# Kernel optimization log

Hardware: AMD Instinct MI355X
Metric: run time of the kernel (lower is better)

Reference implementation:

```python
import jax, jax.numpy as jnp
import numpy as np

B, N, M, D, NH, HD = 2, 1024, 1024, 1536, 16, 96
RD = HD // 3  # per-axis rotary dim = 32
EPS = 1e-6
SCALE = HD ** -0.5


def _rmsnorm(y, w):
    return y * jax.lax.rsqrt(jnp.mean(y * y, axis=-1, keepdims=True) + EPS) * w


def _rope_tables(T, H, W):
    # inv_freqs identical for t/h/w since all three dims are RD
    inv_f = 1.0 / (10000.0 ** (jnp.arange(0, RD, 2, dtype=jnp.float32)[: RD // 2] / RD))
    gt, gh, gw = jnp.meshgrid(
        jnp.arange(T, dtype=jnp.float32),
        jnp.arange(H, dtype=jnp.float32),
        jnp.arange(W, dtype=jnp.float32),
        indexing='ij')
    ft = gt.reshape(-1, 1) * inv_f[None, :]  # [L, RD//2]
    fh = gh.reshape(-1, 1) * inv_f[None, :]
    fw = gw.reshape(-1, 1) * inv_f[None, :]
    return (jnp.cos(ft), jnp.sin(ft), jnp.cos(fh), jnp.sin(fh), jnp.cos(fw), jnp.sin(fw))


def _apply_rope(xq, cos, sin):
    # xq: [B, L, NH, RD]; cos/sin: [L, RD//2]
    c = jnp.concatenate([cos, cos], axis=-1)[None, :, None, :]
    s = jnp.concatenate([sin, sin], axis=-1)[None, :, None, :]
    x1, x2 = jnp.split(xq, 2, axis=-1)
    rot = jnp.concatenate([-x2, x1], axis=-1)
    return xq * c + rot * s


def setup_inputs() -> dict:
    key = jax.random.key(0)
    ks = jax.random.split(key, 10)
    w = lambda k: jax.random.normal(k, (D, D), dtype=jnp.float32) * 0.02
    return {
        'cond': jax.random.normal(ks[0], (B, N, D), dtype=jnp.float32),
        'x': jax.random.normal(ks[1], (B, M, D), dtype=jnp.float32),
        'cond_q_w': w(ks[2]), 'cond_k_w': w(ks[3]), 'cond_v_w': w(ks[4]),
        'cond_qnorm_w': jnp.ones((D,), jnp.float32),
        'cond_knorm_w': jnp.ones((D,), jnp.float32),
        'cond_proj_w': w(ks[5]),
        'x_q_w': w(ks[6]), 'x_k_w': w(ks[7]), 'x_v_w': w(ks[8]),
        'x_qnorm_w': jnp.ones((D,), jnp.float32),
        'x_knorm_w': jnp.ones((D,), jnp.float32),
        'x_proj_w': w(ks[9]),
        'T': 2, 'H': 32, 'W': 32,
    }


def reference(cond, x, cond_q_w, cond_k_w, cond_v_w, cond_qnorm_w, cond_knorm_w,
              cond_proj_w, x_q_w, x_k_w, x_v_w, x_qnorm_w, x_knorm_w, x_proj_w,
              T, H, W):
    # dual-stream QKV + RMSNorm (qkv_bias=False, eval -> no dropout)
    cq = _rmsnorm(cond @ cond_q_w, cond_qnorm_w).reshape(B, N, NH, HD)
    ck = _rmsnorm(cond @ cond_k_w, cond_knorm_w).reshape(B, N, NH, HD)
    cv = (cond @ cond_v_w).reshape(B, N, NH, HD)
    xq = _rmsnorm(x @ x_q_w, x_qnorm_w).reshape(B, M, NH, HD)
    xk = _rmsnorm(x @ x_k_w, x_knorm_w).reshape(B, M, NH, HD)
    xv = (x @ x_v_w).reshape(B, M, NH, HD)

    q = jnp.concatenate([cq, xq], axis=1)  # [B, N+M, NH, HD]
    k = jnp.concatenate([ck, xk], axis=1)
    v = jnp.concatenate([cv, xv], axis=1)

    # 3D RoPE: split head_dim into t/h/w thirds and rotate each with its own freqs
    cos_t, sin_t, cos_h, sin_h, cos_w, sin_w = _rope_tables(T, H, W)
    qt, qh, qw = jnp.split(q, 3, axis=-1)
    kt, kh, kw = jnp.split(k, 3, axis=-1)
    q = jnp.concatenate([_apply_rope(qt, cos_t, sin_t),
                         _apply_rope(qh, cos_h, sin_h),
                         _apply_rope(qw, cos_w, sin_w)], axis=-1)
    k = jnp.concatenate([_apply_rope(kt, cos_t, sin_t),
                         _apply_rope(kh, cos_h, sin_h),
                         _apply_rope(kw, cos_w, sin_w)], axis=-1)

    # joint non-causal SDPA
    scores = jnp.einsum('blhd,bmhd->bhlm', q, k) * SCALE
    attn = jax.nn.softmax(scores, axis=-1)
    out = jnp.einsum('bhlm,bmhd->blhd', attn, v).reshape(B, N + M, D)

    cond_out = out[:, :N] @ cond_proj_w
    x_out = out[:, N:] @ x_proj_w
    return cond_out, x_out
```

## Files before the change

### kernel.cpp

```cpp
#include <hip/hip_runtime.h>
#include <stdint.h>

#define DEV __device__ __forceinline__

using f32x4  = __attribute__((ext_vector_type(4))) float;
using f32x16 = __attribute__((ext_vector_type(16))) float;
using bf16x8 = __attribute__((ext_vector_type(8))) short;

DEV ushort f2bf(float f){
  uint32_t u = __float_as_uint(f);
  u += 0x7FFFu + ((u >> 16) & 1u);
  return (ushort)(u >> 16);
}
DEV float bf2f(ushort h){ return __uint_as_float(((uint32_t)h) << 16); }

DEV void async16(const void* g, void* l){
  __builtin_amdgcn_global_load_lds(
      (const __attribute__((address_space(1))) void*)g,
      (__attribute__((address_space(3))) void*)l, 16, 0, 0);
}

union FU { uint4 u; bf16x8 v; };
DEV bf16x8 as_bf16x8(uint a, uint b, uint c, uint d){ FU f; f.u = make_uint4(a,b,c,d); return f.v; }

__global__ __launch_bounds__(256) void k_conv_in(const float* __restrict__ src, ushort* __restrict__ dst){
  int i = (blockIdx.x * 256 + threadIdx.x) * 8;
  float4 a = *(const float4*)(src + i);
  float4 b = *(const float4*)(src + i + 4);
  union { ushort s[8]; uint4 q; } o;
  o.s[0]=f2bf(a.x); o.s[1]=f2bf(a.y); o.s[2]=f2bf(a.z); o.s[3]=f2bf(a.w);
  o.s[4]=f2bf(b.x); o.s[5]=f2bf(b.y); o.s[6]=f2bf(b.z); o.s[7]=f2bf(b.w);
  *(uint4*)(dst + i) = o.q;
}

__global__ __launch_bounds__(256) void k_transpose_w(
    const float* w0, const float* w1, const float* w2, const float* w3,
    const float* w4, const float* w5, const float* w6, const float* w7,
    ushort* __restrict__ dst){
  __shared__ float tile[32][33];
  int z = blockIdx.z;
  const float* src = (z==0)?w0:(z==1)?w1:(z==2)?w2:(z==3)?w3:(z==4)?w4:(z==5)?w5:(z==6)?w6:w7;
  int n0 = blockIdx.x * 32;
  int k0 = blockIdx.y * 32;
  int tx = threadIdx.x;
  int ty = threadIdx.y;
  for (int j = 0; j < 4; ++j)
    tile[ty + j*8][tx] = src[(size_t)(k0 + ty + j*8) * 1536 + n0 + tx];
  __syncthreads();
  ushort* d = dst + (size_t)z * 1536 * 1536;
  for (int j = 0; j < 4; ++j){
    int n = n0 + ty + j*8;
    int k = k0 + tx;
    d[(size_t)n * 1536 + k] = f2bf(tile[tx][ty + j*8]);
  }
}

template<bool OUT_BF16>
DEV void gemm_tile(const ushort* __restrict__ A, const ushort* __restrict__ Bt, void* __restrict__ Cp,
                   int K, int lda, int ldb, int ldc, int m0, int n0){
  __shared__ ushort As[8192];
  __shared__ ushort Bs[8192];
  int tid = threadIdx.x;
  int w = tid >> 6, lane = tid & 63;
  int g = lane >> 4, fr = lane & 15;
  int wm = (w >> 1) * 64, wn = (w & 1) * 64;
  f32x4 acc[4][4] = {};
  for (int kt = 0; kt < K; kt += 64){
    __syncthreads();
#pragma unroll
    for (int i = 0; i < 4; ++i){
      int ci = i * 256 + tid;
      int row = ci >> 3, ch = ci & 7;
      int src8 = (ch ^ (row & 7)) * 8;
      async16(A  + (size_t)(m0 + row) * lda + kt + src8, As + (i*256 + w*64) * 8);
      async16(Bt + (size_t)(n0 + row) * ldb + kt + src8, Bs + (i*256 + w*64) * 8);
    }
    __syncthreads();
#pragma unroll
    for (int ks = 0; ks < 2; ++ks){
      bf16x8 af[4], bf[4];
      int cidx = ((ks*4 + g) ^ (fr & 7)) * 8;
#pragma unroll
      for (int mi = 0; mi < 4; ++mi) af[mi] = *(const bf16x8*)(As + (wm + mi*16 + fr) * 64 + cidx);
#pragma unroll
      for (int ni = 0; ni < 4; ++ni) bf[ni] = *(const bf16x8*)(Bs + (wn + ni*16 + fr) * 64 + cidx);
#pragma unroll
      for (int mi = 0; mi < 4; ++mi)
#pragma unroll
        for (int ni = 0; ni < 4; ++ni)
          acc[mi][ni] = __builtin_amdgcn_mfma_f32_16x16x32_bf16(af[mi], bf[ni], acc[mi][ni], 0, 0, 0);
    }
  }
  int cr = (lane >> 4) * 4, cc2 = lane & 15;
#pragma unroll
  for (int mi = 0; mi < 4; ++mi)
#pragma unroll
    for (int ni = 0; ni < 4; ++ni)
#pragma unroll
      for (int r = 0; r < 4; ++r){
        size_t idx = (size_t)(m0 + wm + mi*16 + cr + r) * ldc + (n0 + wn + ni*16 + cc2);
        if (OUT_BF16) ((ushort*)Cp)[idx] = f2bf(acc[mi][ni][r]);
        else          ((float*)Cp)[idx]  = acc[mi][ni][r];
      }
}

__global__ __launch_bounds__(256) void k_gemm_qkv(const ushort* __restrict__ inb, const ushort* __restrict__ Wt,
                                                  ushort* __restrict__ Y){
  int f = blockIdx.x;
  int nid = (f & 7) * 144 + (f >> 3);
  int z = nid / 576; int rr = nid - z * 576;
  int by = rr / 36;  int bx = rr - by * 36;
  gemm_tile<true>(inb + (size_t)z * 2048 * 1536, Wt + (size_t)z * 4608 * 1536,
                  Y + (size_t)z * 2048 * 4608, 1536, 1536, 1536, 4608,
                  by * 128, bx * 128);
}

__global__ __launch_bounds__(256) void k_gemm_proj(const ushort* __restrict__ AO, const ushort* __restrict__ Wtp,
                                                   float* __restrict__ out){
  int f = blockIdx.x;
  int nid = (f & 7) * 48 + (f >> 3);
  int z = nid / 96; int rr = nid - z * 96;
  int by = rr / 12; int bx = rr - by * 12;
  int s = z >> 1, bb = z & 1;
  gemm_tile<false>(AO + (size_t)(bb*2048 + s*1024) * 1536, Wtp + (size_t)s * 1536 * 1536,
                   (void*)(out + (size_t)(s*2048 + bb*1024) * 1536), 1536, 1536, 1536, 1536,
                   by * 128, bx * 128);
}

__global__ __launch_bounds__(256) void k_norm_rope(
    const ushort* __restrict__ Y,
    const float* __restrict__ qn_c, const float* __restrict__ kn_c,
    const float* __restrict__ qn_x, const float* __restrict__ kn_x,
    ushort* __restrict__ Qb, ushort* __restrict__ Kb, ushort* __restrict__ Vb){
  int r = blockIdx.x;
  int z = blockIdx.y;
  const ushort* y = Y + ((size_t)z * 2048 + r) * 4608;
  const float* qw = z ? qn_x : qn_c;
  const float* kw = z ? kn_x : kn_c;
  int b = r >> 10;
  int l = (z << 10) + (r & 1023);
  int tid = threadIdx.x;
  __shared__ float cs[48], sn[48];
  if (tid < 48){
    int axis = tid >> 4, fj = tid & 15;
    int pos = (axis == 0) ? (l >> 10) : ((axis == 1) ? ((l >> 5) & 31) : (l & 31));
    float inv = __expf(-(float)fj * 0.5756462732485114f);
    float a = (float)pos * inv;
    sn[tid] = sinf(a); cs[tid] = cosf(a);
  }
  float yq1[3], yq2[3], yk1[3], yk2[3];
  float ssq = 0.f, ssk = 0.f;
#pragma unroll
  for (int i = 0; i < 3; ++i){
    int p = tid + i*256;
    int head = p / 48, rem = p % 48;
    int c1 = head*96 + (rem >> 4)*32 + (rem & 15);
    float a1 = bf2f(y[c1]),        a2 = bf2f(y[c1 + 16]);
    float b1 = bf2f(y[1536 + c1]), b2 = bf2f(y[1536 + c1 + 16]);
    yq1[i]=a1; yq2[i]=a2; yk1[i]=b1; yk2[i]=b2;
    ssq += a1*a1 + a2*a2;
    ssk += b1*b1 + b2*b2;
  }
#pragma unroll
  for (int mm = 1; mm < 64; mm <<= 1){
    ssq += __shfl_xor(ssq, mm);
    ssk += __shfl_xor(ssk, mm);
  }
  __shared__ float red[8];
  int w = tid >> 6;
  if ((tid & 63) == 0){ red[w] = ssq; red[4 + w] = ssk; }
  __syncthreads();
  float scq = rsqrtf((red[0]+red[1]+red[2]+red[3]) * (1.f/1536.f) + 1e-6f);
  float sck = rsqrtf((red[4]+red[5]+red[6]+red[7]) * (1.f/1536.f) + 1e-6f);
  float scqS = scq * 0.1020620726159658f;
#pragma unroll
  for (int i = 0; i < 3; ++i){
    int p = tid + i*256;
    int head = p / 48, rem = p % 48;
    int axis = rem >> 4, fj = rem & 15;
    int c1 = head*96 + axis*32 + fj;
    float c = cs[rem], s = sn[rem];
    size_t rowb = ((size_t)(b*16 + head) * 2048 + l) * 96;
    float a1 = yq1[i] * scqS * qw[c1], a2 = yq2[i] * scqS * qw[c1 + 16];
    Qb[rowb + axis*32 + fj]      = f2bf(a1*c - a2*s);
    Qb[rowb + axis*32 + fj + 16] = f2bf(a2*c + a1*s);
    float b1 = yk1[i] * sck * kw[c1], b2 = yk2[i] * sck * kw[c1 + 16];
    int d1 = axis*32 + fj;
    Kb[rowb + d1]      = f2bf(b1*c - b2*s);
    Kb[rowb + d1 + 16] = f2bf(b2*c + b1*s);
  }
#pragma unroll
  for (int i = 0; i < 6; ++i){
    int cidx = tid + i*256;
    int head = cidx / 96, hd = cidx - head*96;
    Vb[((size_t)(b*16 + head) * 2048 + l) * 96 + hd] = y[3072 + cidx];
  }
}

__global__ __launch_bounds__(256) void k_transpose_v(const ushort* __restrict__ V, ushort* __restrict__ Vt){
  __shared__ ushort t[32][33];
  int bh = blockIdx.z;
  const ushort* src = V + (size_t)bh * 2048 * 96;
  ushort* dst = Vt + (size_t)bh * 96 * 2048;
  int c0 = blockIdx.x * 32;
  int r0 = blockIdx.y * 32;
  int tx = threadIdx.x, ty = threadIdx.y;
  for (int j = 0; j < 4; ++j)
    t[ty + j*8][tx] = src[(size_t)(r0 + ty + j*8) * 96 + c0 + tx];
  __syncthreads();
  for (int j = 0; j < 4; ++j){
    int d = c0 + ty + j*8;
    int l = r0 + tx;
    dst[(size_t)d * 2048 + l] = t[tx][ty + j*8];
  }
}

__global__ __launch_bounds__(256, 2) void k_attn(const ushort* __restrict__ Qb, const ushort* __restrict__ Kb,
                                                 const ushort* __restrict__ Vt, ushort* __restrict__ AO){
  __shared__ ushort Ks[64*100];
  __shared__ ushort Vs[96*68];
  int id = blockIdx.x;
  int nid = (id & 7) * 64 + (id >> 3);
  int qt = nid & 15, bh = nid >> 4;
  int b = bh >> 4, head = bh & 15;
  const ushort* Qh = Qb + (size_t)bh * 2048 * 96;
  const ushort* Kh = Kb + (size_t)bh * 2048 * 96;
  const ushort* Vh = Vt + (size_t)bh * 96 * 2048;
  int tid = threadIdx.x;
  int w = tid >> 6, lane = tid & 63;
  int h = lane >> 5, c = lane & 31;
  int q0 = qt * 128 + w * 32;

  bf16x8 qf[6];
#pragma unroll
  for (int kb = 0; kb < 6; ++kb)
    qf[kb] = *(const bf16x8*)(Qh + (size_t)(q0 + c) * 96 + kb*16 + h*8);

  int gko[3], lko[3], gvo[3], lvo[3];
#pragma unroll
  for (int i = 0; i < 3; ++i){
    int fc = i*256 + tid;
    int krow = (fc * 683) >> 13;
    int kc8  = (fc - krow*12) * 8;
    gko[i] = krow*96 + kc8;
    lko[i] = krow*100 + kc8;
    int vrow = fc >> 3;
    int vc8  = (fc & 7) * 8;
    gvo[i] = vrow*2048 + vc8;
    lvo[i] = vrow*68 + (vc8 ^ ((vrow & 7) << 3));
  }
  uint4 kst[3], vst[3];
#pragma unroll
  for (int i = 0; i < 3; ++i){
    kst[i] = *(const uint4*)(Kh + gko[i]);
    vst[i] = *(const uint4*)(Vh + (size_t)gvo[i]);
  }

  f32x16 o[3] = {};
  float dpart = 0.f;

  for (int kt = 0; kt < 32; ++kt){
#pragma unroll
    for (int i = 0; i < 3; ++i){
      *(uint2*)(Ks + lko[i])     = make_uint2(kst[i].x, kst[i].y);
      *(uint2*)(Ks + lko[i] + 4) = make_uint2(kst[i].z, kst[i].w);
      *(uint2*)(Vs + lvo[i])     = make_uint2(vst[i].x, vst[i].y);
      *(uint2*)(Vs + lvo[i] + 4) = make_uint2(vst[i].z, vst[i].w);
    }
    if (kt + 1 < 32){
#pragma unroll
      for (int i = 0; i < 3; ++i){
        kst[i] = *(const uint4*)(Kh + (kt+1)*6144 + gko[i]);
        vst[i] = *(const uint4*)(Vh + (kt+1)*64 + (size_t)gvo[i]);
      }
    }
    asm volatile("s_waitcnt lgkmcnt(0)" ::: "memory");
    __builtin_amdgcn_s_barrier();
    asm volatile("" ::: "memory");

#pragma unroll
    for (int ni = 0; ni < 2; ++ni){
      f32x16 sa = {};
#pragma unroll
      for (int kb = 0; kb < 6; ++kb){
        const ushort* kp = Ks + (ni*32 + c)*100 + kb*16 + h*8;
        uint2 lo = *(const uint2*)kp;
        uint2 hi = *(const uint2*)(kp + 4);
        sa = __builtin_amdgcn_mfma_f32_32x32x16_bf16(as_bf16x8(lo.x, lo.y, hi.x, hi.y), qf[kb], sa, 0, 0, 0);
      }
      float p[16];
#pragma unroll
      for (int e = 0; e < 16; ++e){
        float x = fmaf(sa[e], 1.44269504f, -14.4269504f);
        asm("v_exp_f32 %0, %1" : "=v"(p[e]) : "v"(x));
      }
      dpart += (((p[0]+p[1])+(p[2]+p[3])) + ((p[4]+p[5])+(p[6]+p[7])))
             + (((p[8]+p[9])+(p[10]+p[11])) + ((p[12]+p[13])+(p[14]+p[15])));
      uint u[8];
#pragma unroll
      for (int e = 0; e < 8; ++e)
        asm("v_cvt_pk_bf16_f32 %0, %1, %2" : "=v"(u[e]) : "v"(p[2*e]), "v"(p[2*e+1]));
      asm("v_permlane32_swap_b32 %0, %1" : "+v"(u[0]), "+v"(u[2]));
      asm("v_permlane32_swap_b32 %0, %1" : "+v"(u[1]), "+v"(u[3]));
      asm("v_permlane32_swap_b32 %0, %1" : "+v"(u[4]), "+v"(u[6]));
      asm("v_permlane32_swap_b32 %0, %1" : "+v"(u[5]), "+v"(u[7]));
      bf16x8 pf0 = as_bf16x8(u[0], u[1], u[2], u[3]);
      bf16x8 pf1 = as_bf16x8(u[4], u[5], u[6], u[7]);
#pragma unroll
      for (int dt = 0; dt < 3; ++dt){
#pragma unroll
        for (int ks = 0; ks < 2; ++ks){
          int chunk = 4*ni + 2*ks + h;
          const ushort* vp = Vs + (dt*32 + c)*68 + ((chunk ^ (c & 7)) << 3);
          uint2 lo = *(const uint2*)vp;
          uint2 hi = *(const uint2*)(vp + 4);
          o[dt] = __builtin_amdgcn_mfma_f32_32x32x16_bf16(ks ? pf1 : pf0,
                    as_bf16x8(lo.x, lo.y, hi.x, hi.y), o[dt], 0, 0, 0);
        }
      }
    }
    asm volatile("" ::: "memory");
    __builtin_amdgcn_s_barrier();
    asm volatile("" ::: "memory");
  }

  float dtot = dpart + __shfl_xor(dpart, 32);
#pragma unroll
  for (int r = 0; r < 16; ++r){
    int qloc = (r & 3) + 8*(r >> 2) + 4*h;
    float den = __shfl(dtot, qloc);
    float dinv = __builtin_amdgcn_rcpf(den);
    size_t rowoff = ((size_t)b * 2048 + q0 + qloc) * 1536 + head * 96;
#pragma unroll
    for (int dt = 0; dt < 3; ++dt){
      float val = o[dt][r] * dinv;
      uint pk; asm("v_cvt_pk_bf16_f32 %0, %1, %2" : "=v"(pk) : "v"(val), "v"(val));
      AO[rowoff + dt*32 + c] = (ushort)pk;
    }
  }
}

extern "C" void kernel_launch(void* const* d_in, const int* in_sizes, int n_in,
                              void* d_out, int out_size, void* d_ws, size_t ws_size,
                              hipStream_t stream){
  const float* cond = (const float*)d_in[0];
  const float* x    = (const float*)d_in[1];
  const float* wq_c = (const float*)d_in[2];
  const float* wk_c = (const float*)d_in[3];
  const float* wv_c = (const float*)d_in[4];
  const float* qn_c = (const float*)d_in[5];
  const float* kn_c = (const float*)d_in[6];
  const float* wp_c = (const float*)d_in[7];
  const float* wq_x = (const float*)d_in[8];
  const float* wk_x = (const float*)d_in[9];
  const float* wv_x = (const float*)d_in[10];
  const float* qn_x = (const float*)d_in[11];
  const float* kn_x = (const float*)d_in[12];
  const float* wp_x = (const float*)d_in[13];

  char* ws = (char*)d_ws;
  ushort* inb = (ushort*)(ws);
  ushort* Wt  = (ushort*)(ws + 12582912ll);
  ushort* Y   = (ushort*)(ws + 50331648ll);
  ushort* Vt  = (ushort*)(ws + 50331648ll);
  ushort* Qb  = (ushort*)(ws + 88080384ll);
  ushort* Kb  = (ushort*)(ws + 100663296ll);
  ushort* Vb  = (ushort*)(ws + 113246208ll);
  ushort* AO  = inb;

  k_conv_in<<<1536, 256, 0, stream>>>(cond, inb);
  k_conv_in<<<1536, 256, 0, stream>>>(x, inb + 3145728);
  k_transpose_w<<<dim3(48,48,8), dim3(32,8), 0, stream>>>(wq_c, wk_c, wv_c, wq_x, wk_x, wv_x, wp_c, wp_x, Wt);
  k_gemm_qkv<<<1152, 256, 0, stream>>>(inb, Wt, Y);
  k_norm_rope<<<dim3(2048,2), 256, 0, stream>>>(Y, qn_c, kn_c, qn_x, kn_x, Qb, Kb, Vb);
  k_transpose_v<<<dim3(3,64,32), dim3(32,8), 0, stream>>>(Vb, Vt);
  k_attn<<<512, 256, 0, stream>>>(Qb, Kb, Vt, AO);
  k_gemm_proj<<<384, 256, 0, stream>>>(AO, Wt + (size_t)9216*1536, (float*)d_out);
  (void)in_sizes; (void)n_in; (void)out_size; (void)ws_size;
}
```

Baseline: 224.4 us.

## Rewrite QKV GEMM with 256x288 tiles, double-buffered LDS and interleaved prefetch

```diff
diff --git a/kernel.cpp b/kernel.cpp
--- a/kernel.cpp
+++ b/kernel.cpp
@@ -55,6 +55,99 @@
   }
 }
 
+__global__ __launch_bounds__(512, 2) void k_gemm_qkv(const ushort* __restrict__ inb,
+                                                     const ushort* __restrict__ Wt,
+                                                     ushort* __restrict__ Y){
+  __shared__ ushort As[2][16384];
+  __shared__ ushort Bs[2][18432];
+  int f = blockIdx.x;
+  int nid = (f & 7) * 32 + (f >> 3);
+  int z = nid >> 7; int r = nid & 127;
+  int my = (r >> 2) & 7, nx = (r >> 5) * 4 + (r & 3);
+  const ushort* A = inb + (size_t)z * 2048 * 1536 + (size_t)(my * 256) * 1536;
+  const ushort* B = Wt  + (size_t)z * 4608 * 1536 + (size_t)(nx * 288) * 1536;
+  ushort* Yt = Y + (size_t)z * 2048 * 4608 + (size_t)(my * 256) * 4608 + nx * 288;
+  int tid = threadIdx.x;
+  int w = tid >> 6, lane = tid & 63;
+  int g = lane >> 4, fr = lane & 15;
+  int wm = (w >> 1) * 64, wn = (w & 1) * 144;
+
+  f32x4 acc[4][9] = {};
+
+  auto stageA = [&](int b, int kt){
+#pragma unroll
+    for (int s = 0; s < 4; ++s){
+      int c = s * 512 + tid;
+      int row = c >> 3, ch = c & 7;
+      async16(A + (size_t)row * 1536 + kt + ((ch ^ (row & 7)) * 8), &As[b][(s*512 + w*64) * 8]);
+    }
+  };
+  auto stageB = [&](int b, int kt){
+#pragma unroll
+    for (int s = 0; s < 4; ++s){
+      int c = s * 512 + tid;
+      int row = c >> 3, ch = c & 7;
+      async16(B + (size_t)row * 1536 + kt + ((ch ^ (row & 7)) * 8), &Bs[b][(s*512 + w*64) * 8]);
+    }
+    if (tid < 256){
+      int c = 2048 + tid;
+      int row = c >> 3, ch = c & 7;
+      async16(B + (size_t)row * 1536 + kt + ((ch ^ (row & 7)) * 8), &Bs[b][(2048 + w*64) * 8]);
+    }
+  };
+
+  stageA(0, 0); stageB(0, 0);
+  asm volatile("s_waitcnt vmcnt(0)" ::: "memory");
+  __builtin_amdgcn_s_barrier();
+  asm volatile("" ::: "memory");
+
+  for (int t = 0; t < 24; ++t){
+    int cur = t & 1; int kt1 = (t + 1) * 64;
+#pragma unroll
+    for (int q = 0; q < 4; ++q){
+      const int ks = q >> 1, mh = q & 1;
+      bf16x8 af[2], bf[9];
+#pragma unroll
+      for (int j = 0; j < 2; ++j){
+        int row = wm + (mh*2 + j)*16 + fr;
+        af[j] = *(const bf16x8*)&As[cur][(row*8 + ((ks*4 + g) ^ (row & 7))) * 8];
+      }
+#pragma unroll
+      for (int ni = 0; ni < 9; ++ni){
+        int row = wn + ni*16 + fr;
+        bf[ni] = *(const bf16x8*)&Bs[cur][(row*8 + ((ks*4 + g) ^ (row & 7))) * 8];
+      }
+      if (t < 23){
+        if (q == 0) stageA(cur ^ 1, kt1);
+        else if (q == 1) stageB(cur ^ 1, kt1);
+      }
+      asm volatile("" ::: "memory");
+      __builtin_amdgcn_s_barrier();
+      asm volatile("" ::: "memory");
+      __builtin_amdgcn_s_setprio(1);
+#pragma unroll
+      for (int ni = 0; ni < 9; ++ni){
+#pragma unroll
+        for (int j = 0; j < 2; ++j)
+          acc[mh*2 + j][ni] = __builtin_amdgcn_mfma_f32_16x16x32_bf16(af[j], bf[ni], acc[mh*2 + j][ni], 0, 0, 0);
+      }
+      __builtin_amdgcn_s_setprio(0);
+      if (q == 3) asm volatile("s_waitcnt vmcnt(0)" ::: "memory");
+      asm volatile("" ::: "memory");
+      __builtin_amdgcn_s_barrier();
+      asm volatile("" ::: "memory");
+    }
+  }
+
+#pragma unroll
+  for (int mi = 0; mi < 4; ++mi)
+#pragma unroll
+    for (int ni = 0; ni < 9; ++ni)
+#pragma unroll
+      for (int rr = 0; rr < 4; ++rr)
+        Yt[(size_t)(wm + mi*16 + g*4 + rr) * 4608 + wn + ni*16 + fr] = f2bf(acc[mi][ni][rr]);
+}
+
 template<bool OUT_BF16>
 DEV void gemm_tile(const ushort* __restrict__ A, const ushort* __restrict__ Bt, void* __restrict__ Cp,
                    int K, int lda, int ldb, int ldc, int m0, int n0){
@@ -102,17 +195,6 @@
         if (OUT_BF16) ((ushort*)Cp)[idx] = f2bf(acc[mi][ni][r]);
         else          ((float*)Cp)[idx]  = acc[mi][ni][r];
       }
-}
-
-__global__ __launch_bounds__(256) void k_gemm_qkv(const ushort* __restrict__ inb, const ushort* __restrict__ Wt,
-                                                  ushort* __restrict__ Y){
-  int f = blockIdx.x;
-  int nid = (f & 7) * 144 + (f >> 3);
-  int z = nid / 576; int rr = nid - z * 576;
-  int by = rr / 36;  int bx = rr - by * 36;
-  gemm_tile<true>(inb + (size_t)z * 2048 * 1536, Wt + (size_t)z * 4608 * 1536,
-                  Y + (size_t)z * 2048 * 4608, 1536, 1536, 1536, 4608,
-                  by * 128, bx * 128);
 }
 
 __global__ __launch_bounds__(256) void k_gemm_proj(const ushort* __restrict__ AO, const ushort* __restrict__ Wtp,
@@ -371,7 +453,7 @@
   k_conv_in<<<1536, 256, 0, stream>>>(cond, inb);
   k_conv_in<<<1536, 256, 0, stream>>>(x, inb + 3145728);
   k_transpose_w<<<dim3(48,48,8), dim3(32,8), 0, stream>>>(wq_c, wk_c, wv_c, wq_x, wk_x, wv_x, wp_c, wp_x, Wt);
-  k_gemm_qkv<<<1152, 256, 0, stream>>>(inb, Wt, Y);
+  k_gemm_qkv<<<256, 512, 0, stream>>>(inb, Wt, Y);
   k_norm_rope<<<dim3(2048,2), 256, 0, stream>>>(Y, qn_c, kn_c, qn_x, kn_x, Qb, Kb, Vb);
   k_transpose_v<<<dim3(3,64,32), dim3(32,8), 0, stream>>>(Vb, Vt);
   k_attn<<<512, 256, 0, stream>>>(Qb, Kb, Vt, AO);
```

Result: faster. 214.7 us (-4.3%).
